# Optimization experiments

Measured on AMD Instinct MI355X. Metric: run time of the kernel, lower is better.

## Reference

```python
import jax, jax.numpy as jnp
import numpy as np

H_WINDOW = 8
X_WINDOW = 8
H_LAG = 0
X_LAG = 0
CHANNELS = 1
B, T = 8192, 2048


def setup_inputs() -> dict:
    key = jax.random.key(0)
    k1, k2, k3 = jax.random.split(key, 3)
    h = jax.random.normal(k1, (B, T, 1), dtype=jnp.float32)
    # torch init: normal(0, 0.05)
    h_weights = 0.05 * jax.random.normal(k2, (H_WINDOW, CHANNELS), dtype=jnp.float32)
    x_weights = 0.05 * jax.random.normal(k3, (X_WINDOW, CHANNELS), dtype=jnp.float32)
    biases = jnp.zeros((1, CHANNELS), dtype=jnp.float32)
    return {"h": h, "h_weights": h_weights, "x_weights": x_weights, "biases": biases}


def reference(h, h_weights, x_weights, biases):
    b, t, _ = h.shape
    start_ix = max(H_WINDOW + H_LAG - 1, X_WINDOW, X_LAG - 1)
    h_t = jnp.transpose(h, (1, 0, 2))              # [T, B, 1] time-major for per-step gather
    hw0 = h[:, :H_WINDOW].reshape(b, H_WINDOW)     # initial h window
    xw0 = jnp.zeros((b, X_WINDOW), dtype=h.dtype)  # initial x window (zeros, as in torch)

    def step(carry, i):
        hw_, xw_ = carry  # [B, H_WINDOW], [B, X_WINDOW]
        out = xw_ @ x_weights + hw_ @ h_weights + biases  # [B, CHANNELS]
        # window updates; at the final step the torch code skips the update but the
        # carry is discarded, so an index-clamped unconditional update is equivalent
        idx = jnp.minimum(i + 1 - H_LAG, t - 1)
        hw_n = jnp.concatenate([hw_, h_t[idx]], axis=1)[:, -H_WINDOW:]
        xw_n = jnp.concatenate([xw_, out], axis=1)[:, -X_WINDOW:]
        return (hw_n, xw_n), out

    _, outs = jax.lax.scan(step, (hw0, xw0), jnp.arange(start_ix, t))  # [T-start_ix, B, C]
    output = jnp.zeros((b, t, CHANNELS), dtype=h.dtype)
    output = output.at[:, start_ix:].set(jnp.transpose(outs, (1, 0, 2)))
    return output
```

## Files before the change

kernel.cpp:

```cpp
#include <hip/hip_runtime.h>


typedef float  f32x4  __attribute__((ext_vector_type(4)));
typedef short  bf16x8 __attribute__((ext_vector_type(8)));

#define TT 2048
#define BB 8192
#define LK 64
#define NTAPS 71
#define LROW 1080

__device__ __forceinline__ unsigned f2bfu(float x) {
    unsigned u = __float_as_uint(x);
    return (u + 0x7FFFu + ((u >> 16) & 1u)) >> 16;
}

__device__ __forceinline__ void group8(const float hwt[8], const float xwt[8],
                                       float bs, const float win[8],
                                       const float nh[8], const float xq[8],
                                       float res[8])
{
#pragma unroll
    for (int u = 0; u < 8; ++u) {
        float acc = bs;
#pragma unroll
        for (int k = u; k < 8; ++k) acc = fmaf(win[k], hwt[k - u], acc);
#pragma unroll
        for (int k = 0; k < u; ++k) acc = fmaf(nh[k], hwt[8 - u + k], acc);
#pragma unroll
        for (int k = u; k < 8; ++k) acc = fmaf(xq[k], xwt[k - u], acc);
#pragma unroll
        for (int k = 0; k < u; ++k) acc = fmaf(res[k], xwt[8 - u + k], acc);
        res[u] = acc;
    }
}

__global__ __launch_bounds__(256) void rr_fused(
    const float* __restrict__ h, const float* __restrict__ hwt_g,
    const float* __restrict__ xwt_g, const float* __restrict__ bias_g,
    float* __restrict__ out)
{
    __shared__ short hlds[16][LROW];
    __shared__ float kl[LK];
    __shared__ float cl[NTAPS + 1];

    const int t   = threadIdx.x;
    const int bid = blockIdx.x;
    const int s   = bid & 1;
    const int r0  = (bid >> 1) << 4;

    const int ts     = s ? 67 : 5;
    const int ntiles = s ? 61 : 62;
    const int gcol0  = s ? 992 : 0;
    const int nf4    = s ? 264 : 268;

    {
        const int row = t >> 4, l16 = t & 15;
        const float* hrow = h + (size_t)(r0 + row) * TT + gcol0;
#pragma unroll
        for (int k = 0; k < 17; ++k) {
            const int c = l16 + 16 * k;
            if (c < nf4) {
                float4 v = reinterpret_cast<const float4*>(hrow)[c];
                uint2 pk;
                pk.x = f2bfu(v.x) | (f2bfu(v.y) << 16);
                pk.y = f2bfu(v.z) | (f2bfu(v.w) << 16);
                *reinterpret_cast<uint2*>(&hlds[row][4 * c]) = pk;
            }
        }
    }

    if (t == 0) {
        float xw[8], hw[8];
#pragma unroll
        for (int j = 0; j < 8; ++j) { xw[j] = xwt_g[j]; hw[j] = hwt_g[j]; }
        float w[8];
#pragma unroll
        for (int j = 0; j < 8; ++j) w[j] = 0.f;
        float ksum = 0.f;
        for (int n = 0; n < LK; ++n) {
            float k;
            if (n == 0) k = 1.f;
            else {
                k = 0.f;
#pragma unroll
                for (int j = 0; j < 8; ++j) k = fmaf(xw[j], w[j], k);
            }
            kl[n] = k; ksum += k;
#pragma unroll
            for (int j = 0; j < 7; ++j) w[j] = w[j + 1];
            w[7] = k;
        }
        float v[8];
#pragma unroll
        for (int j = 0; j < 8; ++j) v[j] = 0.f;
        for (int d = 0; d < NTAPS; ++d) {
            const float nk = (d < LK) ? kl[d] : 0.f;
#pragma unroll
            for (int j = 0; j < 7; ++j) v[j] = v[j + 1];
            v[7] = nk;
            float ca = 0.f;
#pragma unroll
            for (int j = 0; j < 8; ++j) ca = fmaf(hw[j], v[j], ca);
            cl[d] = ca;
        }
        cl[NTAPS] = bias_g[0] * ksum;
    }
    __syncthreads();

    const int lane = t & 63;
    const int v16  = lane & 15;
    const int gq   = lane >> 4;
    const int w    = t >> 6;

    const float biasK = cl[NTAPS];

    bf16x8 bfr[3];
#pragma unroll
    for (int kb = 0; kb < 3; ++kb) {
#pragma unroll
        for (int e = 0; e < 8; ++e) {
            const int idx = 80 + v16 - 32 * kb - 8 * gq - e;
            const float val = (idx >= 0 && idx < NTAPS) ? cl[idx] : 0.f;
            bfr[kb][e] = (short)f2bfu(val);
        }
    }

    for (int tl = w; tl < ntiles; tl += 4) {
        const int colb = 16 * tl;
        f32x4 acc = {0.f, 0.f, 0.f, 0.f};
#pragma unroll
        for (int kb = 0; kb < 3; ++kb) {
            const bf16x8 a = *reinterpret_cast<const bf16x8*>(
                &hlds[v16][colb + 32 * kb + 8 * gq]);
            acc = __builtin_amdgcn_mfma_f32_16x16x32_bf16(a, bfr[kb], acc, 0, 0, 0);
        }
        const int i0 = (ts + tl) * 16;
        float* ob = out + (size_t)(r0 + 4 * gq) * TT + i0 + v16;
#pragma unroll
        for (int q = 0; q < 4; ++q) ob[(size_t)q * TT] = acc[q] + biasK;
    }

    if (s == 0 && t < 16) {
        const float* hr = h + (size_t)(r0 + t) * TT;
        float* orow = out + (size_t)(r0 + t) * TT;
        float hwt[8], xwt[8];
#pragma unroll
        for (int j = 0; j < 8; ++j) { hwt[j] = hwt_g[j]; xwt[j] = xwt_g[j]; }
        const float bs = bias_g[0];
        float win[8], xq[8];
#pragma unroll
        for (int j = 0; j < 8; ++j) { win[j] = hr[j]; xq[j] = 0.f; }
#pragma unroll
        for (int j = 0; j < 8; ++j) orow[j] = 0.f;
        for (int g = 8; g < 80; g += 8) {
            float nh[8], res[8];
#pragma unroll
            for (int j = 0; j < 8; ++j) nh[j] = hr[g + 1 + j];
            group8(hwt, xwt, bs, win, nh, xq, res);
#pragma unroll
            for (int j = 0; j < 8; ++j) orow[g + j] = res[j];
#pragma unroll
            for (int j = 0; j < 8; ++j) { win[j] = nh[j]; xq[j] = res[j]; }
        }
    }
}

extern "C" void kernel_launch(void* const* d_in, const int* in_sizes, int n_in,
                              void* d_out, int out_size, void* d_ws, size_t ws_size,
                              hipStream_t stream) {
    const float* h    = (const float*)d_in[0];
    const float* hwt  = (const float*)d_in[1];
    const float* xwt  = (const float*)d_in[2];
    const float* bias = (const float*)d_in[3];
    float* out = (float*)d_out;
    rr_fused<<<(BB / 16) * 2, 256, 0, stream>>>(h, hwt, xwt, bias, out);
}
```

Before: 35.98 us.

## Split rows into four column segments and parallelize tap precompute across a wavefront

Each 16-row strip is now split into four time segments per block instead of two, doubling the grid and halving shared memory per block so more blocks fit per CU. The serial single-thread computation of the impulse response and convolution taps is moved onto the otherwise idle fourth wavefront, using shuffles for the recurrence and parallel per-tap dot products, so it overlaps the global-to-LDS staging done by the other 192 threads. Conversion to bf16 uses the hardware packed-convert instruction, and the bias is folded into the MFMA accumulator init. The cost is more redundant halo loads and tap precomputation per block.

```diff
diff --git a/kernel.cpp b/kernel.cpp
--- a/kernel.cpp
+++ b/kernel.cpp
@@ -8,7 +8,7 @@
 #define BB 8192
 #define LK 64
 #define NTAPS 71
-#define LROW 1080
+#define LROW 584
 
 __device__ __forceinline__ unsigned f2bfu(float x) {
     unsigned u = __float_as_uint(x);
@@ -46,65 +46,61 @@
 
     const int t   = threadIdx.x;
     const int bid = blockIdx.x;
-    const int s   = bid & 1;
-    const int r0  = (bid >> 1) << 4;
+    const int s   = bid & 3;
+    const int r0  = (bid >> 2) << 4;
 
-    const int ts     = s ? 67 : 5;
-    const int ntiles = s ? 61 : 62;
-    const int gcol0  = s ? 992 : 0;
-    const int nf4    = s ? 264 : 268;
+    const int ts     = (s < 3) ? (5 + 31 * s) : 98;
+    const int ntiles = (s < 3) ? 31 : 30;
+    const int gcol0  = 16 * ts - 80;
+    const int nf4    = (s < 3) ? 144 : 140;
 
-    {
-        const int row = t >> 4, l16 = t & 15;
+    if (t < 192) {
+        const int row = t / 12;
+        const int l12 = t - row * 12;
         const float* hrow = h + (size_t)(r0 + row) * TT + gcol0;
-#pragma unroll
-        for (int k = 0; k < 17; ++k) {
-            const int c = l16 + 16 * k;
+#pragma unroll 4
+        for (int k = 0; k < 12; ++k) {
+            const int c = l12 + 12 * k;
             if (c < nf4) {
                 float4 v = reinterpret_cast<const float4*>(hrow)[c];
                 uint2 pk;
-                pk.x = f2bfu(v.x) | (f2bfu(v.y) << 16);
-                pk.y = f2bfu(v.z) | (f2bfu(v.w) << 16);
+                asm("v_cvt_pk_bf16_f32 %0, %1, %2" : "=v"(pk.x) : "v"(v.x), "v"(v.y));
+                asm("v_cvt_pk_bf16_f32 %0, %1, %2" : "=v"(pk.y) : "v"(v.z), "v"(v.w));
                 *reinterpret_cast<uint2*>(&hlds[row][4 * c]) = pk;
             }
         }
-    }
-
-    if (t == 0) {
-        float xw[8], hw[8];
+    } else {
+        const int l = t - 192;
+        const float xw = (l < 8) ? xwt_g[l] : 0.f;
+        float w = 0.f, ksum = 0.f;
+        for (int n = 0; n < LK; ++n) {
+            float p = xw * w;
+            p += __shfl_xor(p, 1);
+            p += __shfl_xor(p, 2);
+            p += __shfl_xor(p, 4);
+            const float k = (n == 0) ? 1.f : p;
+            ksum += k;
+            if (l == 7) kl[n] = k;
+            const float wshift = __shfl_down(w, 1);
+            w = (l == 7) ? k : wshift;
+        }
+        if (l == 0) cl[NTAPS] = bias_g[0] * ksum;
+        float hw[8];
 #pragma unroll
-        for (int j = 0; j < 8; ++j) { xw[j] = xwt_g[j]; hw[j] = hwt_g[j]; }
-        float w[8];
+        for (int j = 0; j < 8; ++j) hw[j] = hwt_g[j];
 #pragma unroll
-        for (int j = 0; j < 8; ++j) w[j] = 0.f;
-        float ksum = 0.f;
-        for (int n = 0; n < LK; ++n) {
-            float k;
-            if (n == 0) k = 1.f;
-            else {
-                k = 0.f;
+        for (int pass = 0; pass < 2; ++pass) {
+            const int d = l + 64 * pass;
+            if (d < NTAPS) {
+                float ca = 0.f;
 #pragma unroll
-                for (int j = 0; j < 8; ++j) k = fmaf(xw[j], w[j], k);
+                for (int j = 0; j < 8; ++j) {
+                    const int n = d - 7 + j;
+                    if (n >= 0 && n < LK) ca = fmaf(hw[j], kl[n], ca);
+                }
+                cl[d] = ca;
             }
-            kl[n] = k; ksum += k;
-#pragma unroll
-            for (int j = 0; j < 7; ++j) w[j] = w[j + 1];
-            w[7] = k;
         }
-        float v[8];
-#pragma unroll
-        for (int j = 0; j < 8; ++j) v[j] = 0.f;
-        for (int d = 0; d < NTAPS; ++d) {
-            const float nk = (d < LK) ? kl[d] : 0.f;
-#pragma unroll
-            for (int j = 0; j < 7; ++j) v[j] = v[j + 1];
-            v[7] = nk;
-            float ca = 0.f;
-#pragma unroll
-            for (int j = 0; j < 8; ++j) ca = fmaf(hw[j], v[j], ca);
-            cl[d] = ca;
-        }
-        cl[NTAPS] = bias_g[0] * ksum;
     }
     __syncthreads();
 
@@ -128,7 +124,7 @@
 
     for (int tl = w; tl < ntiles; tl += 4) {
         const int colb = 16 * tl;
-        f32x4 acc = {0.f, 0.f, 0.f, 0.f};
+        f32x4 acc = {biasK, biasK, biasK, biasK};
 #pragma unroll
         for (int kb = 0; kb < 3; ++kb) {
             const bf16x8 a = *reinterpret_cast<const bf16x8*>(
@@ -138,7 +134,7 @@
         const int i0 = (ts + tl) * 16;
         float* ob = out + (size_t)(r0 + 4 * gq) * TT + i0 + v16;
 #pragma unroll
-        for (int q = 0; q < 4; ++q) ob[(size_t)q * TT] = acc[q] + biasK;
+        for (int q = 0; q < 4; ++q) ob[(size_t)q * TT] = acc[q];
     }
 
     if (s == 0 && t < 16) {
@@ -174,5 +170,5 @@
     const float* xwt  = (const float*)d_in[2];
     const float* bias = (const float*)d_in[3];
     float* out = (float*)d_out;
-    rr_fused<<<(BB / 16) * 2, 256, 0, stream>>>(h, hwt, xwt, bias, out);
+    rr_fused<<<(BB / 16) * 4, 256, 0, stream>>>(h, hwt, xwt, bias, out);
 }
```

After: 31.44 us. 1.14x faster.
